# Performance work log

Hardware: AMD Instinct MI355X
Metric: run time of the kernel (lower is better)

The kernel has to match this reference:

```python
import jax, jax.numpy as jnp
import numpy as np

N = 50000
E = 800000
IN_C = 256
H1 = 64
H2 = 64
OUT_C = 32
HEADS = 7
NEG_SLOPE = 0.2


def _gat_layer(x, src, dst, W, a_src, a_dst, b, heads, ch, n_nodes):
    # x: [N, F_in]; W: [F_in, heads*ch]; a_src/a_dst: [heads, ch]; b: [heads*ch]
    h = (x @ W).reshape(n_nodes, heads, ch)                      # [N, H, C]
    alpha_s = jnp.einsum('nhc,hc->nh', h, a_src)                 # [N, H]
    alpha_d = jnp.einsum('nhc,hc->nh', h, a_dst)                 # [N, H]
    e = jax.nn.leaky_relu(alpha_s[src] + alpha_d[dst], NEG_SLOPE)  # [E, H]
    # segment softmax grouped by destination node
    m = jax.ops.segment_max(e, dst, num_segments=n_nodes)        # [N, H]
    e = jnp.exp(e - m[dst])
    denom = jax.ops.segment_sum(e, dst, num_segments=n_nodes)    # [N, H]
    alpha = e / (denom[dst] + 1e-16)                             # [E, H]
    msg = h[src] * alpha[:, :, None]                             # [E, H, C]
    out = jax.ops.segment_sum(msg, dst, num_segments=n_nodes)    # [N, H, C]
    return out.reshape(n_nodes, heads * ch) + b


def setup_inputs() -> dict:
    key = jax.random.key(0)
    ks = jax.random.split(key, 16)
    x = jax.random.normal(ks[0], (N, IN_C), dtype=jnp.float32)
    edge_index = jax.random.randint(ks[1], (2, E), 0, N, dtype=jnp.int32)

    def glorot(k, shape):
        fan = shape[0] + shape[-1]
        return jax.random.normal(k, shape, dtype=jnp.float32) * jnp.sqrt(2.0 / fan)

    W1 = glorot(ks[2], (IN_C, HEADS * H1))
    a1_src = glorot(ks[3], (HEADS, H1))
    a1_dst = glorot(ks[4], (HEADS, H1))
    b1 = jnp.zeros((HEADS * H1,), jnp.float32)

    W2 = glorot(ks[5], (HEADS * H1, HEADS * H2))
    a2_src = glorot(ks[6], (HEADS, H2))
    a2_dst = glorot(ks[7], (HEADS, H2))
    b2 = jnp.zeros((HEADS * H2,), jnp.float32)

    W3 = glorot(ks[8], (HEADS * H2, 1 * OUT_C))
    a3_src = glorot(ks[9], (1, OUT_C))
    a3_dst = glorot(ks[10], (1, OUT_C))
    b3 = jnp.zeros((OUT_C,), jnp.float32)

    return {"x": x, "edge_index": edge_index,
            "W1": W1, "a1_src": a1_src, "a1_dst": a1_dst, "b1": b1,
            "W2": W2, "a2_src": a2_src, "a2_dst": a2_dst, "b2": b2,
            "W3": W3, "a3_src": a3_src, "a3_dst": a3_dst, "b3": b3}


def reference(x, edge_index, W1, a1_src, a1_dst, b1, W2, a2_src, a2_dst, b2,
              W3, a3_src, a3_dst, b3):
    # PyG GATConv adds self-loops by default
    loops = jnp.arange(N, dtype=edge_index.dtype)
    src = jnp.concatenate([edge_index[0], loops])
    dst = jnp.concatenate([edge_index[1], loops])
    # dropout is identity in eval mode
    h = _gat_layer(x, src, dst, W1, a1_src, a1_dst, b1, HEADS, H1, N)
    h = jax.nn.relu(h)
    h = _gat_layer(h, src, dst, W2, a2_src, a2_dst, b2, HEADS, H2, N)
    h = jax.nn.relu(h)
    h = _gat_layer(h, src, dst, W3, a3_src, a3_dst, b3, 1, OUT_C, N)
    return jax.nn.log_softmax(h, axis=1)
```

## Files before the change

kernel.cpp:

```cpp
#include <hip/hip_runtime.h>
#include <hip/hip_bf16.h>
#include <hip/hip_fp16.h>

#define NN 50000
#define NP 50176
#define EE 800000
#define ET (EE + NN)
#define NB_SCAN ((NN + 255) / 256)

typedef __attribute__((ext_vector_type(8))) short bf16x8;
typedef __attribute__((ext_vector_type(4))) float f32x4;
typedef __attribute__((ext_vector_type(2))) float f32x2;

static __device__ __forceinline__ float bf2f(__hip_bfloat16 x) { return __bfloat162float(x); }
static __device__ __forceinline__ ushort f2bu(float f) {
    union { __hip_bfloat16 b; ushort u; } c;
    c.b = __float2bfloat16(f);
    return c.u;
}
static __device__ __forceinline__ float u2f(ushort u) {
    union { ushort u; __hip_bfloat16 b; } c;
    c.u = u;
    return __bfloat162float(c.b);
}
static __device__ __forceinline__ unsigned char f2fp8(float v) {
    int p = __builtin_amdgcn_cvt_pk_fp8_f32(v, v, 0, false);
    return (unsigned char)(p & 0xff);
}
static __device__ __forceinline__ void fp8acc_pk(unsigned v, f32x2 w2, f32x2& a01, f32x2& a23) {
#if __has_builtin(__builtin_amdgcn_cvt_pk_f32_fp8)
    f32x2 f01 = __builtin_amdgcn_cvt_pk_f32_fp8((int)v, false);
    f32x2 f23 = __builtin_amdgcn_cvt_pk_f32_fp8((int)v, true);
#else
    f32x2 f01 = { __builtin_amdgcn_cvt_f32_fp8(v, 0), __builtin_amdgcn_cvt_f32_fp8(v, 1) };
    f32x2 f23 = { __builtin_amdgcn_cvt_f32_fp8(v, 2), __builtin_amdgcn_cvt_f32_fp8(v, 3) };
#endif
    asm("v_pk_fma_f32 %0, %1, %2, %0" : "+v"(a01) : "v"(f01), "v"(w2));
    asm("v_pk_fma_f32 %0, %1, %2, %0" : "+v"(a23) : "v"(f23), "v"(w2));
}
static __device__ __forceinline__ void gl2lds(const ushort* g, ushort* l) {
    __builtin_amdgcn_global_load_lds(
        (const __attribute__((address_space(1))) void*)g,
        (__attribute__((address_space(3))) void*)l,
        16, 0, 0);
}

#define PA1 (256 * 448)
#define PA2 (448 * 448)
#define PA3 (448 * 32)
#define PXQ (NN * 64)
#define PTOT (PA1 + PA2 + PA3 + PXQ)
#define PBLK ((PTOT + 255) / 256)
#define CBLK ((ET + 255) / 256)

__global__ void gat_prepcnt_kernel(const float* __restrict__ W1, const float* __restrict__ W2,
                                   const float* __restrict__ W3, const float* __restrict__ x,
                                   ushort* __restrict__ Wt1, ushort* __restrict__ Wt2,
                                   ushort* __restrict__ Wt3, ushort* __restrict__ xb,
                                   const int* __restrict__ ei, int* __restrict__ cnt) {
    int b = blockIdx.x;
    if (b >= PBLK) {
        int i = (b - PBLK) * 256 + threadIdx.x;
        if (i < ET) {
            int dst = (i < EE) ? ei[EE + i] : (i - EE);
            atomicAdd(&cnt[dst], 1);
        }
        return;
    }
    int i = b * 256 + threadIdx.x;
    if (i < PA1) {
        int k = i / 448, n = i - k * 448;
        Wt1[(size_t)n * 256 + k] = f2bu(W1[i]);
        return;
    }
    i -= PA1;
    if (i < PA2) {
        int k = i / 448, n = i - k * 448;
        Wt2[(size_t)n * 448 + k] = f2bu(W2[i]);
        return;
    }
    i -= PA2;
    if (i < PA3) {
        int k = i / 32, n = i - k * 32;
        Wt3[(size_t)n * 448 + k] = f2bu(W3[i]);
        return;
    }
    i -= PA3;
    if (i < PXQ) {
        float4 f = ((const float4*)x)[i];
        ushort u[4] = {f2bu(f.x), f2bu(f.y), f2bu(f.z), f2bu(f.w)};
        ((uint2*)xb)[i] = *(const uint2*)u;
    }
}

__global__ void gat_scan1_kernel(const int* __restrict__ cnt, int* __restrict__ tmp,
                                 int* __restrict__ part) {
    __shared__ int sm[256];
    int tid = threadIdx.x;
    int i = blockIdx.x * 256 + tid;
    int v = (i < NN) ? cnt[i] : 0;
    sm[tid] = v;
    __syncthreads();
    for (int o = 1; o < 256; o <<= 1) {
        int t = (tid >= o) ? sm[tid - o] : 0;
        __syncthreads();
        sm[tid] += t;
        __syncthreads();
    }
    if (i < NN) tmp[i] = sm[tid];
    if (tid == 255) part[blockIdx.x] = sm[255];
}

__global__ void gat_scan2_kernel(int* __restrict__ part) {
    __shared__ int sm[256];
    int tid = threadIdx.x;
    int v = (tid < NB_SCAN) ? part[tid] : 0;
    sm[tid] = v;
    __syncthreads();
    for (int o = 1; o < 256; o <<= 1) {
        int t = (tid >= o) ? sm[tid - o] : 0;
        __syncthreads();
        sm[tid] += t;
        __syncthreads();
    }
    part[tid] = sm[tid];
}

__global__ void gat_scan3_kernel(const int* __restrict__ tmp, const int* __restrict__ part,
                                 int* __restrict__ row_ptr) {
    int i = blockIdx.x * 256 + threadIdx.x;
    int off = (blockIdx.x > 0) ? part[blockIdx.x - 1] : 0;
    if (i < NN) row_ptr[i + 1] = tmp[i] + off;
    if (i == 0) row_ptr[0] = 0;
}

__global__ void gat_fill_kernel(const int* __restrict__ ei, const int* __restrict__ row_ptr,
                                int* __restrict__ fillc, int* __restrict__ colA) {
    int i = blockIdx.x * blockDim.x + threadIdx.x;
    if (i >= ET) return;
    int s, d;
    if (i < EE) { s = ei[i]; d = ei[EE + i]; }
    else        { s = d = i - EE; }
    int pos = row_ptr[d] + atomicAdd(&fillc[d], 1);
    colA[pos] = s;
}

#define GBN 64
#define GBK 32

template <int RF, int DOA, int OM>
__global__ __launch_bounds__(256) void gat_gemm_kernel(
    const ushort* __restrict__ A, const ushort* __restrict__ Wt,
    void* __restrict__ Cv,
    const float* __restrict__ Asrc, const float* __restrict__ Adst,
    float* __restrict__ as8, float* __restrict__ ad8,
    int M, int K, int N) {
    constexpr int GBM = RF * 64;
    constexpr int MT = NP / GBM;
    __shared__ __align__(16) ushort As[2][GBM * GBK];
    __shared__ __align__(16) ushort Bs[2][GBN * GBK];
    int tid = threadIdx.x;
    int wave = tid >> 6, lane = tid & 63;
    int lrow = lane & 15, lq = lane >> 4;

    int mt, head;
    if constexpr (DOA == 1) {
        int id = blockIdx.x;
        int xcd = id & 7, r = id >> 3;
        int g = r / 7;
        head = r - g * 7;
        mt = xcd + g * 8;
        if (mt >= MT) return;
    } else {
        mt = blockIdx.x;
        head = blockIdx.y;
    }
    int m0 = mt * GBM, n0 = head * GBN;

    int srow = lane >> 2, schunk = (lane & 3) * 8;
    f32x4 acc[RF][4] = {};

    int KT = K / GBK;
    {
#pragma unroll
        for (int q = 0; q < RF; q++) {
            const ushort* gp = A + (size_t)(m0 + wave * RF * 16 + q * 16 + srow) * K + schunk;
            gl2lds(gp, &As[0][(wave * RF * 16 + q * 16) * GBK]);
        }
        const ushort* gb = Wt + (size_t)(n0 + wave * 16 + srow) * K + schunk;
        gl2lds(gb, &Bs[0][wave * 16 * GBK]);
    }
    for (int kt = 0; kt < KT; kt++) {
        __syncthreads();
        if (kt + 1 < KT) {
            int nb = (kt + 1) & 1, k0 = (kt + 1) * GBK;
#pragma unroll
            for (int q = 0; q < RF; q++) {
                const ushort* gp = A + (size_t)(m0 + wave * RF * 16 + q * 16 + srow) * K + k0 + schunk;
                gl2lds(gp, &As[nb][(wave * RF * 16 + q * 16) * GBK]);
            }
            const ushort* gb = Wt + (size_t)(n0 + wave * 16 + srow) * K + k0 + schunk;
            gl2lds(gb, &Bs[nb][wave * 16 * GBK]);
        }
        int b = kt & 1;
        bf16x8 af[RF];
#pragma unroll
        for (int rf = 0; rf < RF; rf++)
            af[rf] = *(const bf16x8*)&As[b][(wave * RF * 16 + rf * 16 + lrow) * GBK + lq * 8];
#pragma unroll
        for (int ng = 0; ng < 4; ng++) {
            bf16x8 bf = *(const bf16x8*)&Bs[b][(ng * 16 + lrow) * GBK + lq * 8];
#pragma unroll
            for (int rf = 0; rf < RF; rf++)
                acc[rf][ng] = __builtin_amdgcn_mfma_f32_16x16x32_bf16(af[rf], bf, acc[rf][ng], 0, 0, 0);
        }
    }
#pragma unroll
    for (int rf = 0; rf < RF; rf++)
#pragma unroll
        for (int ng = 0; ng < 4; ng++)
#pragma unroll
            for (int r = 0; r < 4; r++) {
                int row = m0 + wave * RF * 16 + rf * 16 + lq * 4 + r;
                int colI = n0 + ng * 16 + lrow;
                if (row < M && colI < N) {
                    if constexpr (OM == 0)
                        ((__hip_bfloat16*)Cv)[(size_t)row * N + colI] = __float2bfloat16(acc[rf][ng][r]);
                    else
                        ((unsigned char*)Cv)[(size_t)row * N + colI] = f2fp8(acc[rf][ng][r]);
                }
            }
    if constexpr (DOA == 1) {
        float as_l[4], ad_l[4];
#pragma unroll
        for (int ng = 0; ng < 4; ng++) {
            as_l[ng] = Asrc[head * 64 + ng * 16 + lrow];
            ad_l[ng] = Adst[head * 64 + ng * 16 + lrow];
        }
#pragma unroll
        for (int rf = 0; rf < RF; rf++)
#pragma unroll
            for (int r = 0; r < 4; r++) {
                float ps = 0.f, pd = 0.f;
#pragma unroll
                for (int ng = 0; ng < 4; ng++) {
                    ps += acc[rf][ng][r] * as_l[ng];
                    pd += acc[rf][ng][r] * ad_l[ng];
                }
#pragma unroll
                for (int o = 1; o < 16; o <<= 1) {
                    ps += __shfl_xor(ps, o);
                    pd += __shfl_xor(pd, o);
                }
                int row = m0 + wave * RF * 16 + rf * 16 + lq * 4 + r;
                if (lrow == 0 && row < M) {
                    as8[(size_t)row * 8 + head] = ps;
                    ad8[(size_t)row * 8 + head] = pd;
                }
            }
    } else if constexpr (DOA == 2) {
        float as_l[2], ad_l[2];
#pragma unroll
        for (int ng = 0; ng < 2; ng++) {
            as_l[ng] = Asrc[ng * 16 + lrow];
            ad_l[ng] = Adst[ng * 16 + lrow];
        }
#pragma unroll
        for (int rf = 0; rf < RF; rf++)
#pragma unroll
            for (int r = 0; r < 4; r++) {
                float ps = acc[rf][0][r] * as_l[0] + acc[rf][1][r] * as_l[1];
                float pd = acc[rf][0][r] * ad_l[0] + acc[rf][1][r] * ad_l[1];
#pragma unroll
                for (int o = 1; o < 16; o <<= 1) {
                    ps += __shfl_xor(ps, o);
                    pd += __shfl_xor(pd, o);
                }
                int row = m0 + wave * RF * 16 + rf * 16 + lq * 4 + r;
                if (lrow == 0 && row < M) {
                    as8[(size_t)row * 8] = ps;
                    ad8[(size_t)row * 8] = pd;
                }
            }
    }
}

__global__ void gat_aggC7_kernel(const int* __restrict__ rp, const int* __restrict__ colA,
                                 const float* __restrict__ as8, const float* __restrict__ ad8,
                                 const unsigned char* __restrict__ h8,
                                 const float* __restrict__ bias,
                                 __hip_bfloat16* __restrict__ outp) {
    int d = blockIdx.x * 4 + (threadIdx.x >> 6);
    if (d >= NN) return;
    int lane = threadIdx.x & 63;
    int lc = (lane < 56) ? lane : 55;
    unsigned hh = (unsigned)(lc >> 3);
    unsigned lb = (unsigned)lc * 8u;
    float adh = ad8[(size_t)d * 8 + hh];
    int s0 = rp[d], s1 = rp[d + 1];
    int s1m1 = s1 - 1;
    f32x2 a01 = {0.f, 0.f}, a23 = {0.f, 0.f}, a45 = {0.f, 0.f}, a67 = {0.f, 0.f};
    float den = 0.f;

#define GATHER4(B4, ASV, HV) do {                                      \
        _Pragma("unroll")                                              \
        for (int k_ = 0; k_ < 4; k_++) {                               \
            unsigned s_ = (unsigned)__builtin_amdgcn_readlane(myIdx, (B4) + k_); \
            ASV[k_] = as8[s_ * 8u + hh];                               \
            HV[k_] = *(const uint2*)(h8 + (s_ * 448u + lb));           \
        }                                                              \
    } while (0)

#define CONSUME(ASV, HV, JJ) do {                                      \
        float w_[4];                                                   \
        _Pragma("unroll")                                              \
        for (int k_ = 0; k_ < 4; k_++) {                               \
            float e_ = ASV[k_] + adh;                                  \
            e_ = (e_ > 0.f) ? e_ : 0.2f * e_;                          \
            float ww_ = __expf(e_);                                    \
            ww_ = ((JJ) + k_ < s1) ? ww_ : 0.f;                        \
            w_[k_] = ww_;                                              \
            den += ww_;                                                \
        }                                                              \
        _Pragma("unroll")                                              \
        for (int k_ = 0; k_ < 4; k_++) {                               \
            f32x2 w2_ = {w_[k_], w_[k_]};                              \
            fp8acc_pk(HV[k_].x, w2_, a01, a23);                        \
            fp8acc_pk(HV[k_].y, w2_, a45, a67);                        \
        }                                                              \
    } while (0)

    for (int base = s0; base < s1; base += 64) {
        int myIdx = colA[(unsigned)min(base + lane, s1m1)];
        int cnt = min(s1 - base, 64);
        int nb = (cnt + 3) >> 2;
        int jb = base;
        int b4 = 0;
        float as0v[4], as1v[4];
        uint2 hv0[4], hv1[4];
        GATHER4(0, as0v, hv0);
        int rem = nb - 1;
        while (rem >= 2) {
            GATHER4(b4 + 4, as1v, hv1); CONSUME(as0v, hv0, jb); jb += 4;
            GATHER4(b4 + 8, as0v, hv0); CONSUME(as1v, hv1, jb); jb += 4;
            b4 += 8; rem -= 2;
        }
        if (rem == 1) {
            GATHER4(b4 + 4, as1v, hv1); CONSUME(as0v, hv0, jb); jb += 4;
            CONSUME(as1v, hv1, jb);
        } else {
            CONSUME(as0v, hv0, jb);
        }
    }
#undef GATHER4
#undef CONSUME

    float inv = 1.f / (den + 1e-16f);
    const float4* bp = (const float4*)(bias + lb);
    float4 bb0 = bp[0], bb1 = bp[1];
    float bv[8] = {bb0.x, bb0.y, bb0.z, bb0.w, bb1.x, bb1.y, bb1.z, bb1.w};
    float av[8] = {a01.x, a01.y, a23.x, a23.y, a45.x, a45.y, a67.x, a67.y};
    ushort o8[8];
#pragma unroll
    for (int k = 0; k < 8; k++) {
        float o = av[k] * inv + bv[k];
        o = fmaxf(o, 0.f);
        o8[k] = f2bu(o);
    }
    if (lane < 56)
        *(uint4*)((ushort*)outp + (size_t)d * 448 + lane * 8) = *(const uint4*)o8;
}

__global__ void gat_aggCF_kernel(const int* __restrict__ rp, const int* __restrict__ colA,
                                 const float* __restrict__ as8, const float* __restrict__ ad8,
                                 const __hip_bfloat16* __restrict__ h,
                                 const float* __restrict__ bias,
                                 float* __restrict__ outp) {
    int wid = blockIdx.x * 4 + (threadIdx.x >> 6);
    int lane = threadIdx.x & 63;
    int half = lane >> 5;
    unsigned c = (unsigned)(lane & 31);
    int dreal = wid * 2 + half;
    bool valid = dreal < NN;
    int d = valid ? dreal : (NN - 1);
    float adh = ad8[(size_t)d * 8];
    int s0 = rp[d], s1 = rp[d + 1];
    float acc = 0.f, den = 0.f;
    int j = s0;
    for (; j + 2 <= s1; j += 2) {
        unsigned ju = (unsigned)j;
        unsigned sA = (unsigned)colA[ju];
        unsigned sB = (unsigned)colA[ju + 1];
        float eA = as8[sA * 8u] + adh;
        float eB = as8[sB * 8u] + adh;
        float vA = bf2f(h[sA * 32u + c]);
        float vB = bf2f(h[sB * 32u + c]);
        eA = (eA > 0.f) ? eA : 0.2f * eA;
        eB = (eB > 0.f) ? eB : 0.2f * eB;
        float wA = __expf(eA), wB = __expf(eB);
        den += wA + wB;
        acc += wA * vA + wB * vB;
    }
    for (; j < s1; j++) {
        unsigned s = (unsigned)colA[(unsigned)j];
        float e = as8[s * 8u] + adh;
        e = (e > 0.f) ? e : 0.2f * e;
        float w = __expf(e);
        den += w;
        acc += w * bf2f(h[s * 32u + c]);
    }
    float o = acc / (den + 1e-16f) + bias[c];
    float t = o;
#pragma unroll
    for (int off = 16; off > 0; off >>= 1) t = fmaxf(t, __shfl_xor(t, off));
    float ex = __expf(o - t);
#pragma unroll
    for (int off = 16; off > 0; off >>= 1) ex += __shfl_xor(ex, off);
    float res = o - t - __logf(ex);
    if (valid) outp[(size_t)d * 32 + c] = res;
}

extern "C" void kernel_launch(void* const* d_in, const int* in_sizes, int n_in,
                              void* d_out, int out_size, void* d_ws, size_t ws_size,
                              hipStream_t stream) {
    const float* x   = (const float*)d_in[0];
    const int*   ei  = (const int*)d_in[1];
    const float* W1  = (const float*)d_in[2];
    const float* a1s = (const float*)d_in[3];
    const float* a1d = (const float*)d_in[4];
    const float* b1  = (const float*)d_in[5];
    const float* W2  = (const float*)d_in[6];
    const float* a2s = (const float*)d_in[7];
    const float* a2d = (const float*)d_in[8];
    const float* b2  = (const float*)d_in[9];
    const float* W3  = (const float*)d_in[10];
    const float* a3s = (const float*)d_in[11];
    const float* a3d = (const float*)d_in[12];
    const float* b3  = (const float*)d_in[13];
    float* out = (float*)d_out;

    char* w = (char*)d_ws;
    unsigned char* hbuf8 = (unsigned char*)w;
    __hip_bfloat16* hbuf3 = (__hip_bfloat16*)w;
    ushort* xb = (ushort*)(w + (size_t)NP * 448);
    __hip_bfloat16* act = (__hip_bfloat16*)(xb + (size_t)NP * 256);
    float* as8 = (float*)(act + (size_t)NP * 448);
    float* ad8 = as8 + (size_t)NN * 8;
    int* cnt     = (int*)(ad8 + (size_t)NN * 8);
    int* fillc   = cnt + NN;
    int* row_ptr = fillc + NN;
    int* tmp     = row_ptr + (NN + 4);
    int* part    = tmp + NN;
    int* colA    = part + 256;
    char* pw = (char*)(colA + ET);
    pw = (char*)(((uintptr_t)pw + 15) & ~(uintptr_t)15);
    ushort* Wt1 = (ushort*)pw;
    ushort* Wt2 = Wt1 + 448 * 256;
    ushort* Wt3 = Wt2 + 448 * 448;

    hipMemsetAsync(cnt, 0, 2 * (size_t)NN * sizeof(int), stream);

    gat_prepcnt_kernel<<<PBLK + CBLK, 256, 0, stream>>>(W1, W2, W3, x, Wt1, Wt2, Wt3, xb, ei, cnt);
    gat_scan1_kernel<<<NB_SCAN, 256, 0, stream>>>(cnt, tmp, part);
    gat_scan2_kernel<<<1, 256, 0, stream>>>(part);
    gat_scan3_kernel<<<NB_SCAN, 256, 0, stream>>>(tmp, part, row_ptr);
    gat_fill_kernel<<<CBLK, 256, 0, stream>>>(ei, row_ptr, fillc, colA);

    dim3 gemmBlk(256);
    int swzBlocks = 8 * ((196 + 7) / 8) * 7;
    int mtiles1 = NP / 64;
    int aggBlocks = (NN + 3) / 4;

    gat_gemm_kernel<4, 1, 1><<<swzBlocks, gemmBlk, 0, stream>>>(
        xb, Wt1, hbuf8, a1s, a1d, as8, ad8, NN, 256, 448);
    gat_aggC7_kernel<<<aggBlocks, 256, 0, stream>>>(row_ptr, colA, as8, ad8, hbuf8, b1, act);

    gat_gemm_kernel<4, 1, 1><<<swzBlocks, gemmBlk, 0, stream>>>(
        (const ushort*)act, Wt2, hbuf8, a2s, a2d, as8, ad8, NN, 448, 448);
    gat_aggC7_kernel<<<aggBlocks, 256, 0, stream>>>(row_ptr, colA, as8, ad8, hbuf8, b2, act);

    gat_gemm_kernel<1, 2, 0><<<dim3(mtiles1, 1), gemmBlk, 0, stream>>>(
        (const ushort*)act, Wt3, hbuf3, a3s, a3d, as8, ad8, NN, 448, 32);
    int fBlocks = (NN + 7) / 8;
    gat_aggCF_kernel<<<fBlocks, 256, 0, stream>>>(row_ptr, colA, as8, ad8, hbuf3, b3, out);
}
```

Before: 463.9 us.

## Split 7-head aggregation into per-head blocks with 8 nodes per wave

The aggregation kernel for the 7-head layers is restructured. It used one wave per destination node covering all 448 channels. Now each block handles one head for 32 destination nodes, and each 8-lane group owns one node's 64 channels of that head. Edges are gathered in batches of 8 through shuffles, and the column-index load and output store are made nontemporal. This removes the 8 idle lanes per wave and evens out work across nodes of different degree, but it re-reads the edge list and row pointers once per head and launches about 12.5k blocks, one of every 8 exiting at once.

```diff
diff --git a/kernel.cpp b/kernel.cpp
--- a/kernel.cpp
+++ b/kernel.cpp
@@ -7,10 +7,12 @@
 #define EE 800000
 #define ET (EE + NN)
 #define NB_SCAN ((NN + 255) / 256)
+#define AGG_GRPS 1563
 
 typedef __attribute__((ext_vector_type(8))) short bf16x8;
 typedef __attribute__((ext_vector_type(4))) float f32x4;
 typedef __attribute__((ext_vector_type(2))) float f32x2;
+typedef __attribute__((ext_vector_type(4))) unsigned int u32x4;
 
 static __device__ __forceinline__ float bf2f(__hip_bfloat16 x) { return __bfloat162float(x); }
 static __device__ __forceinline__ ushort f2bu(float f) {
@@ -285,78 +287,56 @@
     }
 }
 
-__global__ void gat_aggC7_kernel(const int* __restrict__ rp, const int* __restrict__ colA,
-                                 const float* __restrict__ as8, const float* __restrict__ ad8,
-                                 const unsigned char* __restrict__ h8,
-                                 const float* __restrict__ bias,
-                                 __hip_bfloat16* __restrict__ outp) {
-    int d = blockIdx.x * 4 + (threadIdx.x >> 6);
-    if (d >= NN) return;
-    int lane = threadIdx.x & 63;
-    int lc = (lane < 56) ? lane : 55;
-    unsigned hh = (unsigned)(lc >> 3);
-    unsigned lb = (unsigned)lc * 8u;
-    float adh = ad8[(size_t)d * 8 + hh];
-    int s0 = rp[d], s1 = rp[d + 1];
+__global__ void gat_aggC7s_kernel(const int* __restrict__ rp, const int* __restrict__ colA,
+                                  const float* __restrict__ as8, const float* __restrict__ ad8,
+                                  const unsigned char* __restrict__ h8,
+                                  const float* __restrict__ bias,
+                                  __hip_bfloat16* __restrict__ outp) {
+    int id = blockIdx.x;
+    int slot = id & 7;
+    if (slot >= 7) return;
+    int head = slot;
+    int grp = id >> 3;
+    if (grp >= AGG_GRPS) return;
+    int tid = threadIdx.x;
+    int wave = tid >> 6, lane = tid & 63;
+    int g = lane >> 3, g8 = lane & 7;
+    int gbase = lane & 56;
+    int d = grp * 32 + wave * 8 + g;
+    bool vd = d < NN;
+    int dd = vd ? d : NN - 1;
+    unsigned ch0 = (unsigned)head * 64u + (unsigned)g8 * 8u;
+    float adh = ad8[(size_t)dd * 8 + head];
+    int s0 = rp[dd], s1 = rp[dd + 1];
     int s1m1 = s1 - 1;
     f32x2 a01 = {0.f, 0.f}, a23 = {0.f, 0.f}, a45 = {0.f, 0.f}, a67 = {0.f, 0.f};
     float den = 0.f;
 
-#define GATHER4(B4, ASV, HV) do {                                      \
-        _Pragma("unroll")                                              \
-        for (int k_ = 0; k_ < 4; k_++) {                               \
-            unsigned s_ = (unsigned)__builtin_amdgcn_readlane(myIdx, (B4) + k_); \
-            ASV[k_] = as8[s_ * 8u + hh];                               \
-            HV[k_] = *(const uint2*)(h8 + (s_ * 448u + lb));           \
-        }                                                              \
-    } while (0)
-
-#define CONSUME(ASV, HV, JJ) do {                                      \
-        float w_[4];                                                   \
-        _Pragma("unroll")                                              \
-        for (int k_ = 0; k_ < 4; k_++) {                               \
-            float e_ = ASV[k_] + adh;                                  \
-            e_ = (e_ > 0.f) ? e_ : 0.2f * e_;                          \
-            float ww_ = __expf(e_);                                    \
-            ww_ = ((JJ) + k_ < s1) ? ww_ : 0.f;                        \
-            w_[k_] = ww_;                                              \
-            den += ww_;                                                \
-        }                                                              \
-        _Pragma("unroll")                                              \
-        for (int k_ = 0; k_ < 4; k_++) {                               \
-            f32x2 w2_ = {w_[k_], w_[k_]};                              \
-            fp8acc_pk(HV[k_].x, w2_, a01, a23);                        \
-            fp8acc_pk(HV[k_].y, w2_, a45, a67);                        \
-        }                                                              \
-    } while (0)
-
-    for (int base = s0; base < s1; base += 64) {
-        int myIdx = colA[(unsigned)min(base + lane, s1m1)];
-        int cnt = min(s1 - base, 64);
-        int nb = (cnt + 3) >> 2;
-        int jb = base;
-        int b4 = 0;
-        float as0v[4], as1v[4];
-        uint2 hv0[4], hv1[4];
-        GATHER4(0, as0v, hv0);
-        int rem = nb - 1;
-        while (rem >= 2) {
-            GATHER4(b4 + 4, as1v, hv1); CONSUME(as0v, hv0, jb); jb += 4;
-            GATHER4(b4 + 8, as0v, hv0); CONSUME(as1v, hv1, jb); jb += 4;
-            b4 += 8; rem -= 2;
-        }
-        if (rem == 1) {
-            GATHER4(b4 + 4, as1v, hv1); CONSUME(as0v, hv0, jb); jb += 4;
-            CONSUME(as1v, hv1, jb);
-        } else {
-            CONSUME(as0v, hv0, jb);
-        }
-    }
-#undef GATHER4
-#undef CONSUME
+    for (int base = s0; base < s1; base += 8) {
+        int idxv = __builtin_nontemporal_load(colA + (unsigned)min(base + g8, s1m1));
+        float asv[8];
+        uint2 hv[8];
+#pragma unroll
+        for (int k = 0; k < 8; k++) {
+            unsigned s_ = (unsigned)__shfl(idxv, gbase + k);
+            asv[k] = as8[s_ * 8u + (unsigned)head];
+            hv[k] = *(const uint2*)(h8 + (s_ * 448u + ch0));
+        }
+#pragma unroll
+        for (int k = 0; k < 8; k++) {
+            float e = asv[k] + adh;
+            e = (e > 0.f) ? e : 0.2f * e;
+            float w = __expf(e);
+            w = (base + k < s1) ? w : 0.f;
+            den += w;
+            f32x2 w2 = {w, w};
+            fp8acc_pk(hv[k].x, w2, a01, a23);
+            fp8acc_pk(hv[k].y, w2, a45, a67);
+        }
+    }
 
     float inv = 1.f / (den + 1e-16f);
-    const float4* bp = (const float4*)(bias + lb);
+    const float4* bp = (const float4*)(bias + ch0);
     float4 bb0 = bp[0], bb1 = bp[1];
     float bv[8] = {bb0.x, bb0.y, bb0.z, bb0.w, bb1.x, bb1.y, bb1.z, bb1.w};
     float av[8] = {a01.x, a01.y, a23.x, a23.y, a45.x, a45.y, a67.x, a67.y};
@@ -367,8 +347,10 @@
         o = fmaxf(o, 0.f);
         o8[k] = f2bu(o);
     }
-    if (lane < 56)
-        *(uint4*)((ushort*)outp + (size_t)d * 448 + lane * 8) = *(const uint4*)o8;
+    if (vd) {
+        u32x4 ov = *(const u32x4*)o8;
+        __builtin_nontemporal_store(ov, (u32x4*)((ushort*)outp + (size_t)d * 448 + ch0));
+    }
 }
 
 __global__ void gat_aggCF_kernel(const int* __restrict__ rp, const int* __restrict__ colA,
@@ -469,15 +451,15 @@
     dim3 gemmBlk(256);
     int swzBlocks = 8 * ((196 + 7) / 8) * 7;
     int mtiles1 = NP / 64;
-    int aggBlocks = (NN + 3) / 4;
+    int aggBlocksS = 8 * AGG_GRPS;
 
     gat_gemm_kernel<4, 1, 1><<<swzBlocks, gemmBlk, 0, stream>>>(
         xb, Wt1, hbuf8, a1s, a1d, as8, ad8, NN, 256, 448);
-    gat_aggC7_kernel<<<aggBlocks, 256, 0, stream>>>(row_ptr, colA, as8, ad8, hbuf8, b1, act);
+    gat_aggC7s_kernel<<<aggBlocksS, 256, 0, stream>>>(row_ptr, colA, as8, ad8, hbuf8, b1, act);
 
     gat_gemm_kernel<4, 1, 1><<<swzBlocks, gemmBlk, 0, stream>>>(
         (const ushort*)act, Wt2, hbuf8, a2s, a2d, as8, ad8, NN, 448, 448);
-    gat_aggC7_kernel<<<aggBlocks, 256, 0, stream>>>(row_ptr, colA, as8, ad8, hbuf8, b2, act);
+    gat_aggC7s_kernel<<<aggBlocksS, 256, 0, stream>>>(row_ptr, colA, as8, ad8, hbuf8, b2, act);
 
     gat_gemm_kernel<1, 2, 0><<<dim3(mtiles1, 1), gemmBlk, 0, stream>>>(
         (const ushort*)act, Wt3, hbuf3, a3s, a3d, as8, ad8, NN, 448, 32);
```

After: 593.3 us. 1.28x slower.
